# Kernel tuning notes

Measured on AMD Instinct MI355X. Metric: run time of the kernel, lower is better.

Reference implementation:

```python
import jax, jax.numpy as jnp
import numpy as np

EPS_LN = 1e-5

def layer_norm(x, w, b):
    u = x.mean(-1, keepdims=True)
    s = jnp.mean((x - u) ** 2, -1, keepdims=True)
    return w * ((x - u) / jnp.sqrt(s + EPS_LN)) + b

def mlp(x, W, b, lw, lb):
    return jax.nn.relu(layer_norm(x @ W + b, lw, lb))

def mlp_gate(x, W, b, lw, lb):
    return jax.nn.sigmoid(layer_norm(x @ W + b, lw, lb))

def setup_inputs() -> dict:
    N, D = 768, 64
    key = jax.random.key(0)
    ks = jax.random.split(key, 12)
    inp = {
        'corr_index': jax.random.normal(ks[0], (N, N, 2), jnp.float32),
        'nei_index': jax.random.randint(ks[1], (N, N), 0, 2).astype(jnp.int64),
        'nei_num': jax.random.randint(ks[2], (N,), 0, N).astype(jnp.int64),
        'hidden_state': jax.random.normal(ks[3], (N, D), jnp.float32),
        'agent_v': jax.random.normal(ks[4], (N, 2), jnp.float32),
        # relativeLayer: MLP(3, D)
        'rel_w': jax.random.normal(ks[5], (3, D), jnp.float32) * (1.0 / np.sqrt(3)),
        'rel_b': jnp.zeros((D,), jnp.float32),
        'rel_lw': jnp.ones((D,), jnp.float32),
        'rel_lb': jnp.zeros((D,), jnp.float32),
        # ngate: MLP_gate(3D, D)
        'ng_w': jax.random.normal(ks[6], (3 * D, D), jnp.float32) * (1.0 / np.sqrt(3 * D)),
        'ng_b': jnp.zeros((D,), jnp.float32),
        'ng_lw': jnp.ones((D,), jnp.float32),
        'ng_lb': jnp.zeros((D,), jnp.float32),
        # WAr: MLP(3D, 1) -- LayerNorm(1) is identity in the source
        'war_w': jax.random.normal(ks[7], (3 * D, 1), jnp.float32) * (1.0 / np.sqrt(3 * D)),
        'war_b': jnp.zeros((1,), jnp.float32),
        # weight: MLP(D, D)
        'wt_w': jax.random.normal(ks[8], (D, D), jnp.float32) * (1.0 / np.sqrt(D)),
        'wt_b': jnp.zeros((D,), jnp.float32),
        'wt_lw': jnp.ones((D,), jnp.float32),
        'wt_lb': jnp.zeros((D,), jnp.float32),
    }
    return inp

def reference(corr_index, nei_index, nei_num, hidden_state, agent_v,
              rel_w, rel_b, rel_lw, rel_lb,
              ng_w, ng_b, ng_lw, ng_lb,
              war_w, war_b,
              wt_w, wt_b, wt_lw, wt_lb):
    N, D = hidden_state.shape
    # pair layout: row i*N+j  (i = receiver row of the NxN grid, j = column)
    agent_vt = jnp.tile(agent_v, (N, 1))                     # [N*N, 2], row i*N+j -> agent_v[j]
    corr_t = corr_index.reshape(N * N, 2)
    dot = agent_vt[:, 0] * corr_t[:, 0] + agent_vt[:, 1] * corr_t[:, 1]
    judge = jnp.sum(agent_vt ** 2, -1)
    angle = dot / (jnp.sqrt(judge * jnp.sum(corr_t ** 2, -1)) + 1e-10)
    angle = jnp.where(judge == 0, -1.0, angle)
    corr3 = jnp.concatenate([corr_t, angle[:, None]], -1)    # [N*N, 3]

    r_t = mlp(corr3, rel_w, rel_b, rel_lw, rel_lb)           # [N*N, D]
    nei_inputs = jnp.tile(hidden_state, (N, 1))              # row i*N+j -> h[j]
    hi_t = jnp.repeat(hidden_state, N, axis=0)               # row i*N+j -> h[i]
    tmp = jnp.concatenate([r_t, hi_t, nei_inputs], 1)        # [N*N, 3D]

    mask = (nei_index.reshape(N * N) > 0)
    nGate = mlp_gate(tmp, ng_w, ng_b, ng_lw, ng_lb)          # [N*N, D]
    tt = jax.nn.relu(tmp @ war_w + war_b).reshape(-1)        # LayerNorm(1) == identity

    Pos = jnp.where(mask, tt, 0.0).reshape(N, N)
    Pos = jnp.where(Pos == 0, -10000.0, Pos)
    Pos = jax.nn.softmax(Pos, axis=1)
    Pos_t = Pos.reshape(-1)

    H = jnp.where(mask[:, None], nei_inputs * nGate * Pos_t[:, None], 0.0)
    H_sum = mlp(H.reshape(N, N, D).sum(1), wt_w, wt_b, wt_lw, wt_lb)
    return hidden_state + H_sum
```

## Files before the change

### kernel.cpp

```cpp
#include <hip/hip_runtime.h>
#include <math.h>

#define NN 768
#define DD 64
#define WPB 4
#define HALVES 2
#define JW (NN / HALVES)
#define TPW (JW / 16 / WPB)
#define RSTRIDE 34
#define PREBLKS 18
#define PSTRIDE 68

typedef _Float16 half8 __attribute__((ext_vector_type(8)));
typedef float    f32x4 __attribute__((ext_vector_type(4)));
typedef __fp16   p2f   __attribute__((ext_vector_type(2)));

union FragU { uint4 u4; unsigned int u[4]; half8 h; };
union PkU   { unsigned int u; p2f p; };

__device__ __forceinline__ unsigned int pk2(float a, float b) {
    PkU t; t.p = __builtin_amdgcn_cvt_pkrtz(a, b); return t.u;
}
__device__ __forceinline__ float lane_bcast(float v, int src) {
    return __int_as_float(__builtin_amdgcn_readlane(__float_as_int(v), src));
}
__device__ __forceinline__ float rfl(float v) {
    return __int_as_float(__builtin_amdgcn_readfirstlane(__float_as_int(v)));
}
__device__ __forceinline__ f32x4 mfma16(FragU a, FragU b, f32x4 c) {
    return __builtin_amdgcn_mfma_f32_16x16x32_f16(a.h, b.h, c, 0, 0, 0);
}

__global__ __launch_bounds__(256) void k_prepack(
    const float* __restrict__ hs, const float* __restrict__ ng_w,
    const float* __restrict__ ng_b, const float* __restrict__ war_w,
    const float* __restrict__ war_b,
    const float* __restrict__ rel_w, const float* __restrict__ rel_b,
    const float* __restrict__ rel_lw, const float* __restrict__ rel_lb,
    float* __restrict__ sbase, float* __restrict__ warb, float* __restrict__ war3,
    unsigned int* __restrict__ hf16,
    unsigned int* __restrict__ afragS, unsigned int* __restrict__ afragR,
    float* __restrict__ mom)
{
    const int t = threadIdx.x, blk = blockIdx.x;
    const int lane = t & 63, q = t >> 6, g = lane >> 4, c16 = lane & 15;

    if (blk >= PREBLKS) {
        const int row = (blk - PREBLKS) * 4 + q;
        const float hv = hs[row * DD + lane];
        float a2 = ng_b[lane];
        #pragma unroll 8
        for (int k = 0; k < DD; ++k)
            a2 = fmaf(lane_bcast(hv, k), ng_w[(DD + k) * DD + lane], a2);
        sbase[row * DD + lane] = a2;
        float t2 = hv * war_w[DD + lane];
        float t3 = hv * war_w[2 * DD + lane];
        #pragma unroll
        for (int o = 32; o; o >>= 1) { t2 += __shfl_xor(t2, o); t3 += __shfl_xor(t3, o); }
        if (lane == 0) { warb[row] = t2 + war_b[0]; war3[row] = t3; }
        return;
    }

    for (int idx = blk * 256 + t; idx < NN * 32; idx += PREBLKS * 256) {
        const int row = idx >> 5, c = idx & 31;
        hf16[idx] = pk2(hs[row * DD + 2 * c], hs[row * DD + 2 * c + 1]);
    }

    if (blk < 16) {
        const int b = blk >> 2, c = blk & 3;
        const int dout = 16 * b + c16;
        const int k0 = 32 * c + g * 8 + 2 * q;
        const int r0 = (k0 < 64) ? k0 : (k0 + 64);
        afragS[(blk * 64 + lane) * 4 + q] =
            pk2(ng_w[r0 * DD + dout], ng_w[(r0 + 1) * DD + dout]);
    } else if (blk == 16) {
        const int b = q;
        const int d = 16 * b + c16;
        const float rlwd = rel_lw[d], rlbd = rel_lb[d];
        const float c0 = rel_w[d] * rlwd;
        const float c1 = rel_w[DD + d] * rlwd;
        const float c2 = rel_w[2 * DD + d] * rlwd;
        const float c3 = rel_b[d] * rlwd;
        PkU h01, h23, h45;
        h01.p = __builtin_amdgcn_cvt_pkrtz(c0, c1);
        h23.p = __builtin_amdgcn_cvt_pkrtz(c2, c3);
        h45.p = __builtin_amdgcn_cvt_pkrtz(rlwd, rlbd);
        const unsigned l01 = pk2(c0 - (float)h01.p[0], c1 - (float)h01.p[1]);
        const unsigned l23 = pk2(c2 - (float)h23.p[0], c3 - (float)h23.p[1]);
        const unsigned l45 = pk2(rlwd - (float)h45.p[0], rlbd - (float)h45.p[1]);
        const unsigned int base = (b * 64 + lane) * 4;
        unsigned v0, v1, v2;
        if (g == 0 || g == 1)      { v0 = h01.u; v1 = h23.u; v2 = h45.u; }
        else if (g == 2)           { v0 = l01;   v1 = l23;   v2 = l45;   }
        else                       { v0 = 0u;    v1 = 0u;    v2 = 0u;    }
        afragR[base + 0] = v0;
        afragR[base + 1] = v1;
        afragR[base + 2] = v2;
        afragR[base + 3] = 0u;
    } else {
        if (t < 64) {
            const float x0 = rel_w[t], x1 = rel_w[DD + t], x2 = rel_w[2 * DD + t];
            const float x3 = rel_b[t];
            float v[14] = {x0, x1, x2, x3,
                           x0 * x0, x1 * x1, x2 * x2, x3 * x3,
                           x0 * x1, x0 * x2, x0 * x3, x1 * x2, x1 * x3, x2 * x3};
            #pragma unroll
            for (int qq = 0; qq < 14; ++qq) {
                float s = v[qq];
                #pragma unroll
                for (int o = 32; o; o >>= 1) s += __shfl_xor(s, o);
                if (t == 0) mom[qq] = s * (1.f / 64.f);
            }
        }
    }
}

__global__ __launch_bounds__(64 * WPB) void k_main(
    const float* __restrict__ corr, const int* __restrict__ nei,
    const float* __restrict__ hs, const float* __restrict__ av,
    const float* __restrict__ ng_lw, const float* __restrict__ ng_lb,
    const float* __restrict__ war_w,
    const float* __restrict__ sbase, const float* __restrict__ warb,
    const float* __restrict__ war3,
    const unsigned int* __restrict__ afragS, const unsigned int* __restrict__ afragR,
    const unsigned int* __restrict__ hf16, const float* __restrict__ mom,
    float* __restrict__ part)
{
    const int i = blockIdx.x >> 1;
    const int h = blockIdx.x & 1;
    const int tid = threadIdx.x;
    const int lane = tid & 63, wave = tid >> 6;
    const int g = lane >> 4, c16 = lane & 15;

    __shared__ uint4 sm_aS[16 * 64];
    __shared__ __align__(16) float sm_cst[4 * DD];
    __shared__ unsigned int smr[WPB * 16 * RSTRIDE];
    __shared__ float sm_red[WPB][DD];
    __shared__ float sm_m[WPB], sm_l[WPB];

    for (int f = tid; f < 16 * 64; f += 64 * WPB)
        sm_aS[f] = ((const uint4*)afragS)[f];
    {
        const int a = tid >> 6, d = tid & 63;
        float v;
        if (a == 0)      v = sbase[i * DD + d];
        else if (a == 1) v = war_w[d];
        else if (a == 2) v = ng_lw[d];
        else             v = ng_lb[d];
        sm_cst[a * DD + d] = v;
    }

    FragU aR[4];
    #pragma unroll
    for (int b = 0; b < 4; ++b) aR[b].u4 = ((const uint4*)afragR)[b * 64 + lane];

    const float m0 = rfl(mom[0]), m1 = rfl(mom[1]), m2 = rfl(mom[2]), m3 = rfl(mom[3]);
    const float M00 = rfl(mom[4]), M11 = rfl(mom[5]), M22 = rfl(mom[6]), M33 = rfl(mom[7]);
    const float M01 = rfl(mom[8]), M02 = rfl(mom[9]), M03 = rfl(mom[10]);
    const float M12 = rfl(mom[11]), M13 = rfl(mom[12]), M23 = rfl(mom[13]);
    const float warbase = rfl(warb[i]);

    unsigned int* wrbase = smr + (wave * 16 + c16) * RSTRIDE;

    float acc[16];
    #pragma unroll
    for (int x = 0; x < 16; ++x) acc[x] = 0.f;
    float mrun = -INFINITY, lrun = 0.f;

    __syncthreads();

    const int jbase = h * JW;
    int jj = jbase + 16 * wave + c16;
    float2 cc = ((const float2*)corr)[i * NN + jj];
    float2 vv = ((const float2*)av)[jj];

    unsigned zofs = 0;

    #pragma unroll 1
    for (int t = 0; t < TPW; ++t) {
        asm volatile("" : "+v"(zofs));
        const uint4* aSp = sm_aS + zofs;
        const float* cst = sm_cst + zofs;

        const int    nv = nei[i * NN + jj];
        const float  w3 = war3[jj];
        FragU bx2, bx3;
        bx2.u4 = *(const uint4*)(hf16 + jj * 32 + 4 * g);
        bx3.u4 = *(const uint4*)(hf16 + jj * 32 + 16 + 4 * g);

        const int tn  = (t + 1 < TPW) ? (t + 1) : t;
        const int jjn = jbase + 16 * (wave + WPB * tn) + c16;
        const float2 cc_n = ((const float2*)corr)[i * NN + jjn];
        const float2 vv_n = ((const float2*)av)[jjn];

        const float cx = cc.x, cy = cc.y;
        const float judge = vv.x * vv.x + vv.y * vv.y;
        const float dotv = fmaf(vv.x, cx, vv.y * cy);
        const float cn = cx * cx + cy * cy;
        float angle = __fdividef(dotv, sqrtf(judge * cn) + 1e-10f);
        if (judge == 0.f) angle = -1.f;

        const float u = fmaf(cx, m0, fmaf(cy, m1, fmaf(angle, m2, m3)));
        float e2 = M33;
        e2 = fmaf(cx * cx, M00, e2);
        e2 = fmaf(cy * cy, M11, e2);
        e2 = fmaf(angle * angle, M22, e2);
        e2 = fmaf(2.f * cx, fmaf(cy, M01, fmaf(angle, M02, M03)), e2);
        e2 = fmaf(2.f * cy, fmaf(angle, M12, M13), e2);
        e2 = fmaf(2.f * angle, M23, e2);
        const float vare = (e2 - u * u) + 1e-5f;
        const float inv = rsqrtf(vare);
        const float sig = vare * inv;

        PkU s01, s23, s45;
        s01.p = __builtin_amdgcn_cvt_pkrtz(cx, cy);
        s23.p = __builtin_amdgcn_cvt_pkrtz(angle, 1.f);
        s45.p = __builtin_amdgcn_cvt_pkrtz(-u, sig);
        const unsigned l0 = pk2(cx - (float)s01.p[0], cy - (float)s01.p[1]);
        const unsigned l1 = pk2(angle - (float)s23.p[0], 0.f);
        const unsigned l2 = pk2((-u) - (float)s45.p[0], sig - (float)s45.p[1]);
        FragU b1;
        b1.u[0] = (g == 3) ? 0u : ((g == 1) ? l0 : s01.u);
        b1.u[1] = (g == 3) ? 0u : ((g == 1) ? l1 : s23.u);
        b1.u[2] = (g == 3) ? 0u : ((g == 1) ? l2 : s45.u);
        b1.u[3] = 0u;

        const f32x4 Z = {0.f, 0.f, 0.f, 0.f};
        float wd = 0.f;
        #pragma unroll
        for (int b = 0; b < 4; ++b) {
            const f32x4 P = mfma16(aR[b], b1, Z);
            const f32x4 wv = *(const f32x4*)(cst + 1 * DD + 16 * b + 4 * g);
            const float r0f = fmaxf(P[0], 0.f) * inv;
            const float r1f = fmaxf(P[1], 0.f) * inv;
            const float r2f = fmaxf(P[2], 0.f) * inv;
            const float r3f = fmaxf(P[3], 0.f) * inv;
            wd = fmaf(r0f, wv[0], wd);
            wd = fmaf(r1f, wv[1], wd);
            wd = fmaf(r2f, wv[2], wd);
            wd = fmaf(r3f, wv[3], wd);
            uint2 wvv;
            wvv.x = pk2(r0f, r1f);
            wvv.y = pk2(r2f, r3f);
            *(uint2*)(wrbase + 8 * b + 2 * g) = wvv;
        }

        FragU bx0, bx1;
        {
            const uint2 lo0 = *(const uint2*)(wrbase + 4 * g);
            const uint2 hi0 = *(const uint2*)(wrbase + 4 * g + 2);
            bx0.u[0] = lo0.x; bx0.u[1] = lo0.y; bx0.u[2] = hi0.x; bx0.u[3] = hi0.y;
            const uint2 lo1 = *(const uint2*)(wrbase + 16 + 4 * g);
            const uint2 hi1 = *(const uint2*)(wrbase + 16 + 4 * g + 2);
            bx1.u[0] = lo1.x; bx1.u[1] = lo1.y; bx1.u[2] = hi1.x; bx1.u[3] = hi1.y;
        }

        const f32x4 hv0 = *(const f32x4*)(hs + jj * DD +  0 + 4 * g);
        const f32x4 hv1 = *(const f32x4*)(hs + jj * DD + 16 + 4 * g);
        const f32x4 hv2 = *(const f32x4*)(hs + jj * DD + 32 + 4 * g);
        const f32x4 hv3 = *(const f32x4*)(hs + jj * DD + 48 + 4 * g);

        wd += __shfl_xor(wd, 16);
        wd += __shfl_xor(wd, 32);

        f32x4 S[4];
        #pragma unroll
        for (int b = 0; b < 4; ++b) {
            f32x4 cinit = *(const f32x4*)(cst + 0 * DD + 16 * b + 4 * g);
            FragU a2f, a3f, a0f, a1f;
            a2f.u4 = aSp[(b * 4 + 2) * 64 + lane];
            a3f.u4 = aSp[(b * 4 + 3) * 64 + lane];
            a0f.u4 = aSp[(b * 4 + 0) * 64 + lane];
            a1f.u4 = aSp[(b * 4 + 1) * 64 + lane];
            cinit = mfma16(a2f, bx2, cinit);
            cinit = mfma16(a3f, bx3, cinit);
            cinit = mfma16(a0f, bx0, cinit);
            cinit = mfma16(a1f, bx1, cinit);
            S[b] = cinit;
        }

        float s1 = 0.f, s2 = 0.f;
        #pragma unroll
        for (int x = 0; x < 16; ++x) {
            const float sv = S[x >> 2][x & 3];
            s1 += sv; s2 = fmaf(sv, sv, s2);
        }
        s1 += __shfl_xor(s1, 16); s1 += __shfl_xor(s1, 32);
        s2 += __shfl_xor(s2, 16); s2 += __shfl_xor(s2, 32);
        const float u2 = s1 * (1.f / 64.f);
        const float var2 = fmaf(s2, 1.f / 64.f, -u2 * u2);
        const float inv2 = rsqrtf(var2 + 1e-5f);

        float tt = wd + w3 + warbase;
        tt = fmaxf(tt, 0.f);
        const bool msk = nv > 0;
        const float p = (msk && tt > 0.f) ? tt : -10000.f;

        const float mn = fmaxf(mrun, p);
        const float alpha = __expf(mrun - mn);
        const float e = __expf(p - mn);
        const float eacc = msk ? e : 0.f;
        lrun = fmaf(lrun, alpha, e);
        mrun = mn;

        #pragma unroll
        for (int b = 0; b < 4; ++b) {
            const f32x4 hvb = (b == 0) ? hv0 : (b == 1) ? hv1 : (b == 2) ? hv2 : hv3;
            const f32x4 lw = *(const f32x4*)(cst + 2 * DD + 16 * b + 4 * g);
            const f32x4 lb = *(const f32x4*)(cst + 3 * DD + 16 * b + 4 * g);
            #pragma unroll
            for (int r = 0; r < 4; ++r) {
                const float ngv = fmaf((S[b][r] - u2) * inv2, lw[r], lb[r]);
                const float gate = __fdividef(1.f, 1.f + __expf(-ngv));
                acc[b * 4 + r] = fmaf(acc[b * 4 + r], alpha, eacc * gate * hvb[r]);
            }
        }

        jj = jjn; cc = cc_n; vv = vv_n;
    }

    #pragma unroll
    for (int o = 1; o <= 8; o <<= 1) {
        const float mo  = __shfl_xor(mrun, o);
        const float lo_ = __shfl_xor(lrun, o);
        const float M   = fmaxf(mrun, mo);
        const float a1  = __expf(mrun - M);
        const float a2  = __expf(mo - M);
        lrun = lrun * a1 + lo_ * a2;
        #pragma unroll
        for (int x = 0; x < 16; ++x) {
            const float ao = __shfl_xor(acc[x], o);
            acc[x] = acc[x] * a1 + ao * a2;
        }
        mrun = M;
    }
    if (c16 == 0) {
        #pragma unroll
        for (int b = 0; b < 4; ++b)
            #pragma unroll
            for (int r = 0; r < 4; ++r)
                sm_red[wave][16 * b + g * 4 + r] = acc[b * 4 + r];
        if (lane == 0) { sm_m[wave] = mrun; sm_l[wave] = lrun; }
    }
    __syncthreads();

    if (tid < DD) {
        float M = sm_m[0];
        #pragma unroll
        for (int w = 1; w < WPB; ++w) M = fmaxf(M, sm_m[w]);
        float L = 0.f, A = 0.f;
        #pragma unroll
        for (int w = 0; w < WPB; ++w) {
            const float f = __expf(sm_m[w] - M);
            L = fmaf(sm_l[w], f, L);
            A = fmaf(sm_red[w][tid], f, A);
        }
        float* p = part + (i * HALVES + h) * PSTRIDE;
        p[tid] = A;
        if (tid == 0) { p[64] = M; p[65] = L; }
    }
}

__global__ __launch_bounds__(64) void k_final(
    const float* __restrict__ hs, const float* __restrict__ part,
    const float* __restrict__ wt_w, const float* __restrict__ wt_b,
    const float* __restrict__ wt_lw, const float* __restrict__ wt_lb,
    float* __restrict__ out)
{
    const int i = blockIdx.x;
    const int tid = threadIdx.x;

    const float* p0 = part + (i * HALVES + 0) * PSTRIDE;
    const float* p1 = part + (i * HALVES + 1) * PSTRIDE;
    const float m0 = p0[64], l0 = p0[65];
    const float m1 = p1[64], l1 = p1[65];
    const float M  = fmaxf(m0, m1);
    const float f0 = __expf(m0 - M), f1 = __expf(m1 - M);
    const float L  = l0 * f0 + l1 * f1;
    const float A  = p0[tid] * f0 + p1[tid] * f1;
    const float Hv = A / L;

    float v = wt_b[tid];
    #pragma unroll 8
    for (int k = 0; k < DD; ++k)
        v = fmaf(lane_bcast(Hv, k), wt_w[k * DD + tid], v);
    float t1 = v, t2 = v * v;
    #pragma unroll
    for (int o = 32; o; o >>= 1) { t1 += __shfl_xor(t1, o); t2 += __shfl_xor(t2, o); }
    const float uo = t1 * (1.f / 64.f);
    const float varo = fmaf(t2, 1.f / 64.f, -uo * uo);
    const float invo = rsqrtf(varo + 1e-5f);
    const float ro = fmaf((v - uo) * invo, wt_lw[tid], wt_lb[tid]);
    out[i * DD + tid] = hs[i * DD + tid] + fmaxf(ro, 0.f);
}

extern "C" void kernel_launch(void* const* d_in, const int* in_sizes, int n_in,
                              void* d_out, int out_size, void* d_ws, size_t ws_size,
                              hipStream_t stream) {
    const float* corr   = (const float*)d_in[0];
    const int*   nei    = (const int*)  d_in[1];
    const float* hs     = (const float*)d_in[3];
    const float* av     = (const float*)d_in[4];
    const float* rel_w  = (const float*)d_in[5];
    const float* rel_b  = (const float*)d_in[6];
    const float* rel_lw = (const float*)d_in[7];
    const float* rel_lb = (const float*)d_in[8];
    const float* ng_w   = (const float*)d_in[9];
    const float* ng_b   = (const float*)d_in[10];
    const float* ng_lw  = (const float*)d_in[11];
    const float* ng_lb  = (const float*)d_in[12];
    const float* war_w  = (const float*)d_in[13];
    const float* war_b  = (const float*)d_in[14];
    const float* wt_w   = (const float*)d_in[15];
    const float* wt_b   = (const float*)d_in[16];
    const float* wt_lw  = (const float*)d_in[17];
    const float* wt_lb  = (const float*)d_in[18];
    float* out = (float*)d_out;

    float* ws    = (float*)d_ws;
    float* sbase = ws;
    float* warb  = sbase + NN * DD;
    float* war3  = warb + NN;
    float* mom   = war3 + NN;
    unsigned int* hf16   = (unsigned int*)(mom + 16);
    unsigned int* afragS = hf16 + NN * 32;
    unsigned int* afragR = afragS + 16 * 64 * 4;
    float* part  = (float*)(afragR + 4 * 64 * 4);

    k_prepack<<<PREBLKS + NN / 4, 256, 0, stream>>>(
        hs, ng_w, ng_b, war_w, war_b, rel_w, rel_b, rel_lw, rel_lb,
        sbase, warb, war3, hf16, afragS, afragR, mom);
    k_main<<<NN * HALVES, 64 * WPB, 0, stream>>>(
        corr, nei, hs, av, ng_lw, ng_lb, war_w, sbase, warb, war3,
        afragS, afragR, hf16, mom, part);
    k_final<<<NN, 64, 0, stream>>>(
        hs, part, wt_w, wt_b, wt_lw, wt_lb, out);
}
```

Before: 145.9 us.

## Split rows into three blocks and precompute per-column relative features in LDS

Each row's column range is now split across three blocks instead of two, launched on a 2D grid, and each wave owns 64 contiguous columns. All 64 lanes first compute the angle and layer-norm statistics for their own column in one pass and store hi/lo fp16 split B-fragments to shared memory. The inner loop then reads these fragments instead of computing them on only 16 of 64 lanes. The 1/sigma scale is folded into the MFMA input so the per-output multiply goes away. The final kernel merges three softmax partials, and the change adds more blocks and partial traffic plus extra LDS use.

```diff
diff --git a/kernel.cpp b/kernel.cpp
--- a/kernel.cpp
+++ b/kernel.cpp
@@ -4,10 +4,11 @@
 #define NN 768
 #define DD 64
 #define WPB 4
-#define HALVES 2
+#define HALVES 3
 #define JW (NN / HALVES)
-#define TPW (JW / 16 / WPB)
+#define NSUB 4
 #define RSTRIDE 34
+#define B1STR 12
 #define PREBLKS 18
 #define PSTRIDE 68
 
@@ -126,14 +127,15 @@
     const unsigned int* __restrict__ hf16, const float* __restrict__ mom,
     float* __restrict__ part)
 {
-    const int i = blockIdx.x >> 1;
-    const int h = blockIdx.x & 1;
+    const int h = blockIdx.x;
+    const int i = blockIdx.y;
     const int tid = threadIdx.x;
     const int lane = tid & 63, wave = tid >> 6;
     const int g = lane >> 4, c16 = lane & 15;
 
     __shared__ uint4 sm_aS[16 * 64];
     __shared__ __align__(16) float sm_cst[4 * DD];
+    __shared__ unsigned int sm_b1[WPB * 64 * B1STR];
     __shared__ unsigned int smr[WPB * 16 * RSTRIDE];
     __shared__ float sm_red[WPB][DD];
     __shared__ float sm_m[WPB], sm_l[WPB];
@@ -162,37 +164,13 @@
 
     unsigned int* wrbase = smr + (wave * 16 + c16) * RSTRIDE;
 
-    float acc[16];
-    #pragma unroll
-    for (int x = 0; x < 16; ++x) acc[x] = 0.f;
-    float mrun = -INFINITY, lrun = 0.f;
-
     __syncthreads();
 
-    const int jbase = h * JW;
-    int jj = jbase + 16 * wave + c16;
-    float2 cc = ((const float2*)corr)[i * NN + jj];
-    float2 vv = ((const float2*)av)[jj];
-
-    unsigned zofs = 0;
-
-    #pragma unroll 1
-    for (int t = 0; t < TPW; ++t) {
-        asm volatile("" : "+v"(zofs));
-        const uint4* aSp = sm_aS + zofs;
-        const float* cst = sm_cst + zofs;
-
-        const int    nv = nei[i * NN + jj];
-        const float  w3 = war3[jj];
-        FragU bx2, bx3;
-        bx2.u4 = *(const uint4*)(hf16 + jj * 32 + 4 * g);
-        bx3.u4 = *(const uint4*)(hf16 + jj * 32 + 16 + 4 * g);
-
-        const int tn  = (t + 1 < TPW) ? (t + 1) : t;
-        const int jjn = jbase + 16 * (wave + WPB * tn) + c16;
-        const float2 cc_n = ((const float2*)corr)[i * NN + jjn];
-        const float2 vv_n = ((const float2*)av)[jjn];
-
+    const int jwbase = h * JW + wave * 64;
+    {
+        const int j = jwbase + lane;
+        const float2 cc = ((const float2*)corr)[i * NN + j];
+        const float2 vv = ((const float2*)av)[j];
         const float cx = cc.x, cy = cc.y;
         const float judge = vv.x * vv.x + vv.y * vv.y;
         const float dotv = fmaf(vv.x, cx, vv.y * cy);
@@ -210,20 +188,52 @@
         e2 = fmaf(2.f * angle, M23, e2);
         const float vare = (e2 - u * u) + 1e-5f;
         const float inv = rsqrtf(vare);
-        const float sig = vare * inv;
-
+
+        const float xc0 = cx * inv, xc1 = cy * inv, xc2 = angle * inv;
+        const float xc3 = inv, xc4 = -u * inv;
         PkU s01, s23, s45;
-        s01.p = __builtin_amdgcn_cvt_pkrtz(cx, cy);
-        s23.p = __builtin_amdgcn_cvt_pkrtz(angle, 1.f);
-        s45.p = __builtin_amdgcn_cvt_pkrtz(-u, sig);
-        const unsigned l0 = pk2(cx - (float)s01.p[0], cy - (float)s01.p[1]);
-        const unsigned l1 = pk2(angle - (float)s23.p[0], 0.f);
-        const unsigned l2 = pk2((-u) - (float)s45.p[0], sig - (float)s45.p[1]);
+        s01.p = __builtin_amdgcn_cvt_pkrtz(xc0, xc1);
+        s23.p = __builtin_amdgcn_cvt_pkrtz(xc2, xc3);
+        s45.p = __builtin_amdgcn_cvt_pkrtz(xc4, 1.f);
+        const unsigned l0 = pk2(xc0 - (float)s01.p[0], xc1 - (float)s01.p[1]);
+        const unsigned l1 = pk2(xc2 - (float)s23.p[0], xc3 - (float)s23.p[1]);
+        const unsigned l2 = pk2(xc4 - (float)s45.p[0], 0.f);
+
+        unsigned int* bp = sm_b1 + (wave * 64 + lane) * B1STR;
+        *(uint4*)(bp)     = make_uint4(s01.u, s23.u, s45.u, 0u);
+        *(uint4*)(bp + 4) = make_uint4(l0, l1, l2, 0u);
+    }
+
+    float acc[16];
+    #pragma unroll
+    for (int x = 0; x < 16; ++x) acc[x] = 0.f;
+    float mrun = -INFINITY, lrun = 0.f;
+
+    unsigned zofs = 0;
+
+    #pragma unroll 1
+    for (int s = 0; s < NSUB; ++s) {
+        asm volatile("" : "+v"(zofs));
+        const uint4* aSp = sm_aS + zofs;
+        const float* cst = sm_cst + zofs;
+
+        const int jj = jwbase + 16 * s + c16;
+        const int    nv = nei[i * NN + jj];
+        const float  w3 = war3[jj];
+        FragU bx2, bx3;
+        bx2.u4 = *(const uint4*)(hf16 + jj * 32 + 4 * g);
+        bx3.u4 = *(const uint4*)(hf16 + jj * 32 + 16 + 4 * g);
+
         FragU b1;
-        b1.u[0] = (g == 3) ? 0u : ((g == 1) ? l0 : s01.u);
-        b1.u[1] = (g == 3) ? 0u : ((g == 1) ? l1 : s23.u);
-        b1.u[2] = (g == 3) ? 0u : ((g == 1) ? l2 : s45.u);
-        b1.u[3] = 0u;
+        {
+            const unsigned int* bp =
+                sm_b1 + (wave * 64 + 16 * s + c16) * B1STR + ((g == 1) ? 4 : 0);
+            const uint4 w = *(const uint4*)bp;
+            b1.u[0] = (g == 3) ? 0u : w.x;
+            b1.u[1] = (g == 3) ? 0u : w.y;
+            b1.u[2] = (g == 3) ? 0u : w.z;
+            b1.u[3] = 0u;
+        }
 
         const f32x4 Z = {0.f, 0.f, 0.f, 0.f};
         float wd = 0.f;
@@ -231,10 +241,10 @@
         for (int b = 0; b < 4; ++b) {
             const f32x4 P = mfma16(aR[b], b1, Z);
             const f32x4 wv = *(const f32x4*)(cst + 1 * DD + 16 * b + 4 * g);
-            const float r0f = fmaxf(P[0], 0.f) * inv;
-            const float r1f = fmaxf(P[1], 0.f) * inv;
-            const float r2f = fmaxf(P[2], 0.f) * inv;
-            const float r3f = fmaxf(P[3], 0.f) * inv;
+            const float r0f = fmaxf(P[0], 0.f);
+            const float r1f = fmaxf(P[1], 0.f);
+            const float r2f = fmaxf(P[2], 0.f);
+            const float r3f = fmaxf(P[3], 0.f);
             wd = fmaf(r0f, wv[0], wd);
             wd = fmaf(r1f, wv[1], wd);
             wd = fmaf(r2f, wv[2], wd);
@@ -315,8 +325,6 @@
                 acc[b * 4 + r] = fmaf(acc[b * 4 + r], alpha, eacc * gate * hvb[r]);
             }
         }
-
-        jj = jjn; cc = cc_n; vv = vv_n;
     }
 
     #pragma unroll
@@ -370,14 +378,21 @@
     const int i = blockIdx.x;
     const int tid = threadIdx.x;
 
-    const float* p0 = part + (i * HALVES + 0) * PSTRIDE;
-    const float* p1 = part + (i * HALVES + 1) * PSTRIDE;
-    const float m0 = p0[64], l0 = p0[65];
-    const float m1 = p1[64], l1 = p1[65];
-    const float M  = fmaxf(m0, m1);
-    const float f0 = __expf(m0 - M), f1 = __expf(m1 - M);
-    const float L  = l0 * f0 + l1 * f1;
-    const float A  = p0[tid] * f0 + p1[tid] * f1;
+    float ms[HALVES], ls[HALVES];
+    float M = -INFINITY;
+    #pragma unroll
+    for (int hh = 0; hh < HALVES; ++hh) {
+        const float* p = part + (i * HALVES + hh) * PSTRIDE;
+        ms[hh] = p[64]; ls[hh] = p[65];
+        M = fmaxf(M, ms[hh]);
+    }
+    float L = 0.f, A = 0.f;
+    #pragma unroll
+    for (int hh = 0; hh < HALVES; ++hh) {
+        const float f = __expf(ms[hh] - M);
+        L = fmaf(ls[hh], f, L);
+        A = fmaf(part[(i * HALVES + hh) * PSTRIDE + tid], f, A);
+    }
     const float Hv = A / L;
 
     float v = wt_b[tid];
@@ -430,7 +445,7 @@
     k_prepack<<<PREBLKS + NN / 4, 256, 0, stream>>>(
         hs, ng_w, ng_b, war_w, war_b, rel_w, rel_b, rel_lw, rel_lb,
         sbase, warb, war3, hf16, afragS, afragR, mom);
-    k_main<<<NN * HALVES, 64 * WPB, 0, stream>>>(
+    k_main<<<dim3(HALVES, NN), 64 * WPB, 0, stream>>>(
         corr, nei, hs, av, ng_lw, ng_lb, war_w, sbase, warb, war3,
         afragS, afragR, hf16, mom, part);
     k_final<<<NN, 64, 0, stream>>>(
```

After: 144.9 us. No clear change (-0.7%).
